# Optimization experiments

Hardware: AMD Instinct MI355X
Metric: run time of the kernel (lower is better)

## Reference

```python
import jax, jax.numpy as jnp
import numpy as np

N = 50000      # nodes
E = 800000     # edges (before self loops)
F_IN = 64      # num_features
HID = 64       # hidden_channels
NCLS = 10      # num_classes
NG = 512       # number of graphs in batch
NEG_SLOPE = 0.2


def setup_inputs() -> dict:
    key = jax.random.key(0)
    ks = jax.random.split(key, 14)
    def g(k, shape, scale=0.1):
        return jax.random.normal(k, shape, dtype=jnp.float32) * scale
    inp = {
        "x": jax.random.normal(ks[0], (N, F_IN), dtype=jnp.float32),
        "edge_index": jax.random.randint(ks[1], (2, E), 0, N, dtype=jnp.int64),
        "batch": jnp.sort(jax.random.randint(ks[2], (N,), 0, NG, dtype=jnp.int64)),
        # conv1: GATv2Conv(F_IN, HID, heads=2), separate lin_l / lin_r, att [H, C]
        "Wl1": g(ks[3], (F_IN, 2 * HID)),
        "Wr1": g(ks[4], (F_IN, 2 * HID)),
        "att1": g(ks[5], (2, HID)),
        "b1": g(ks[6], (2 * HID,)),
        # conv2: GATv2Conv(2*HID, HID, heads=1)
        "Wl2": g(ks[7], (2 * HID, HID)),
        "Wr2": g(ks[8], (2 * HID, HID)),
        "att2": g(ks[9], (1, HID)),
        "b2": g(ks[10], (HID,)),
        # final classifier
        "lin_w": g(ks[11], (HID, NCLS)),
        "lin_b": g(ks[12], (NCLS,)),
    }
    return inp


def _gatv2(x, Wl, Wr, att, b, src, dst, n, heads, outc):
    """GATv2Conv: e = a^T LeakyReLU(Wl x_j + Wr x_i), segment-softmax over dst."""
    xl = (x @ Wl).reshape(n, heads, outc)   # source transform
    xr = (x @ Wr).reshape(n, heads, outc)   # target transform
    e = jax.nn.leaky_relu(xl[src] + xr[dst], NEG_SLOPE)      # [E, H, C]
    logits = jnp.einsum('ehc,hc->eh', e, att)                # [E, H]
    m = jax.lax.stop_gradient(jax.ops.segment_max(logits, dst, num_segments=n))
    ex = jnp.exp(logits - m[dst])
    denom = jax.ops.segment_sum(ex, dst, num_segments=n)     # [N, H]
    alpha = ex / denom[dst]                                  # [E, H]
    out = jax.ops.segment_sum(alpha[:, :, None] * xl[src], dst, num_segments=n)
    return out.reshape(n, heads * outc) + b


def reference(x, edge_index, batch, Wl1, Wr1, att1, b1, Wl2, Wr2, att2, b2, lin_w, lin_b):
    n = x.shape[0]
    loop = jnp.arange(n, dtype=edge_index.dtype)
    src = jnp.concatenate([edge_index[0], loop])   # add_self_loops=True
    dst = jnp.concatenate([edge_index[1], loop])
    h = jax.nn.elu(_gatv2(x, Wl1, Wr1, att1, b1, src, dst, n, 2, HID))   # [N, 2*HID]
    h = _gatv2(h, Wl2, Wr2, att2, b2, src, dst, n, 1, HID)               # [N, HID]
    # global mean pool over graph ids
    sums = jax.ops.segment_sum(h, batch, num_segments=NG)                # [NG, HID]
    cnt = jax.ops.segment_sum(jnp.ones((n,), h.dtype), batch, num_segments=NG)
    pooled = sums / jnp.maximum(cnt, 1.0)[:, None]
    # dropout is identity in eval mode
    return pooled @ lin_w + lin_b                                        # [NG, NCLS]
```

## Files before the change

### kernel.cpp

```cpp
#include <hip/hip_runtime.h>
#include <hip/hip_bf16.h>

#define F_IN 64
#define HID 64
#define NCLS 10
#define NG 512

__global__ void gemm1_kernel(const float* __restrict__ x,
                             const float* __restrict__ Wl,
                             const float* __restrict__ Wr,
                             float* __restrict__ xl, float* __restrict__ xr,
                             int N_) {
    __shared__ float xs[8 * 64];
    int r0 = blockIdx.x * 8;
    int t = threadIdx.x;
    for (int i = t; i < 8 * 64; i += 256) {
        int r = i >> 6;
        xs[i] = (r0 + r < N_) ? x[(long)(r0 + r) * 64 + (i & 63)] : 0.f;
    }
    __syncthreads();
    const float* W = (t < 128) ? Wl : Wr;
    int col = t & 127;
    float acc[8] = {0.f, 0.f, 0.f, 0.f, 0.f, 0.f, 0.f, 0.f};
    for (int k = 0; k < 64; ++k) {
        float w = W[k * 128 + col];
#pragma unroll
        for (int r = 0; r < 8; ++r) acc[r] += xs[r * 64 + k] * w;
    }
    float* out = (t < 128) ? xl : xr;
#pragma unroll
    for (int r = 0; r < 8; ++r)
        if (r0 + r < N_) out[(long)(r0 + r) * 128 + col] = acc[r];
}

__global__ void gemm2_kernel(const float* __restrict__ h1,
                             const float* __restrict__ Wl,
                             const float* __restrict__ Wr,
                             float* __restrict__ xl, float* __restrict__ xr,
                             int N_) {
    __shared__ float hs[8 * 128];
    int r0 = blockIdx.x * 8;
    int t = threadIdx.x;
    for (int i = t; i < 8 * 128; i += 128) {
        int r = i >> 7;
        hs[i] = (r0 + r < N_) ? h1[(long)(r0 + r) * 128 + (i & 127)] : 0.f;
    }
    __syncthreads();
    const float* W = (t < 64) ? Wl : Wr;
    int col = t & 63;
    float acc[8] = {0.f, 0.f, 0.f, 0.f, 0.f, 0.f, 0.f, 0.f};
    for (int k = 0; k < 128; ++k) {
        float w = W[k * 64 + col];
#pragma unroll
        for (int r = 0; r < 8; ++r) acc[r] += hs[r * 128 + k] * w;
    }
    float* out = (t < 64) ? xl : xr;
#pragma unroll
    for (int r = 0; r < 8; ++r)
        if (r0 + r < N_) out[(long)(r0 + r) * 64 + col] = acc[r];
}

__global__ void count_kernel(const int* __restrict__ ei, int* __restrict__ deg, int E_) {
    int e = blockIdx.x * 256 + threadIdx.x;
    if (e < E_) atomicAdd(&deg[ei[E_ + e]], 1);
}

__global__ void scan1_kernel(const int* __restrict__ deg, int* __restrict__ rs_part,
                             int* __restrict__ blksum, int N_) {
    __shared__ int tmp[256];
    int t = threadIdx.x;
    int i = blockIdx.x * 256 + t;
    int v = (i < N_) ? deg[i] : 0;
    tmp[t] = v;
    __syncthreads();
    for (int off = 1; off < 256; off <<= 1) {
        int add = (t >= off) ? tmp[t - off] : 0;
        __syncthreads();
        tmp[t] += add;
        __syncthreads();
    }
    if (i < N_) rs_part[i] = tmp[t] - v;
    if (t == 255) blksum[blockIdx.x] = tmp[255];
}

__global__ void scan2_kernel(int* __restrict__ blksum, int nblk) {
    __shared__ int tmp[256];
    int t = threadIdx.x;
    int v = (t < nblk) ? blksum[t] : 0;
    tmp[t] = v;
    __syncthreads();
    for (int off = 1; off < 256; off <<= 1) {
        int add = (t >= off) ? tmp[t - off] : 0;
        __syncthreads();
        tmp[t] += add;
        __syncthreads();
    }
    if (t < nblk) blksum[t] = tmp[t] - v;
}

__global__ void scan3_kernel(const int* __restrict__ rs_part,
                             const int* __restrict__ blksum,
                             int* __restrict__ rs, int* __restrict__ cursor,
                             int N_, int E_) {
    int i = blockIdx.x * 256 + threadIdx.x;
    if (i < N_) {
        int v = rs_part[i] + blksum[blockIdx.x];
        rs[i] = v;
        cursor[i] = v;
    }
    if (i == 0) rs[N_] = E_;
}

__global__ void scatter_kernel(const int* __restrict__ ei, int* __restrict__ cursor,
                               int* __restrict__ csr_src, int E_) {
    int e = blockIdx.x * 256 + threadIdx.x;
    if (e < E_) {
        int d = ei[E_ + e];
        int pos = atomicAdd(&cursor[d], 1);
        csr_src[pos] = ei[e];
    }
}

__global__ void gbound_kernel(const int* __restrict__ batch, int* __restrict__ gstart,
                              int N_) {
    int i = blockIdx.x * 256 + threadIdx.x;
    if (i >= N_) return;
    int bi = batch[i];
    int bprev = (i == 0) ? -1 : batch[i - 1];
    for (int g = bprev + 1; g <= bi; ++g) gstart[g] = i;
    if (i == N_ - 1)
        for (int g = bi + 1; g <= NG; ++g) gstart[g] = N_;
}

__global__ void gat1_kernel(const float* __restrict__ xl,
                            float* __restrict__ xr,
                            const float* __restrict__ att,
                            const float* __restrict__ b1,
                            const int* __restrict__ rs,
                            const int* __restrict__ csr_src,
                            int N_) {
    int wid = (int)(((long)blockIdx.x * blockDim.x + threadIdx.x) >> 6);
    int lane = threadIdx.x & 63;
    if (wid >= N_ * 2) return;
    int d = wid >> 1, h = wid & 1;
    int g = lane >> 4;
    int c4 = lane & 15;
    long rowoff = (long)d * 128 + h * 64 + c4 * 4;
    const float4 xr4 = *(const float4*)(xr + rowoff);
    const float4 at4 = *(const float4*)(att + h * 64 + c4 * 4);

    int k0 = rs[d], k1 = rs[d + 1];
    int cnt = k1 - k0 + 1;

    float4 acc = make_float4(0.f, 0.f, 0.f, 0.f);
    float den = 0.f;
    for (int c0 = 0; c0 < cnt; c0 += 64) {
        int wl = c0 + lane;
        int myidx = (wl >= 1 && wl < cnt) ? csr_src[k0 + wl - 1] : d;
        int lim = min(64, cnt - c0);
        for (int p = 0; p < lim; p += 8) {
            int e0 = p + g, e1 = p + 4 + g;
            int s0 = __shfl(myidx, e0, 64);
            int s1 = __shfl(myidx, e1, 64);
            bool v0 = e0 < lim, v1 = e1 < lim;
            float4 a0 = *(const float4*)(xl + (long)s0 * 128 + h * 64 + c4 * 4);
            float4 a1 = *(const float4*)(xl + (long)s1 * 128 + h * 64 + c4 * 4);
            float t, p0, p1;
            t = a0.x + xr4.x; t = (t >= 0.f) ? t : 0.2f * t; p0  = at4.x * t;
            t = a0.y + xr4.y; t = (t >= 0.f) ? t : 0.2f * t; p0 += at4.y * t;
            t = a0.z + xr4.z; t = (t >= 0.f) ? t : 0.2f * t; p0 += at4.z * t;
            t = a0.w + xr4.w; t = (t >= 0.f) ? t : 0.2f * t; p0 += at4.w * t;
            t = a1.x + xr4.x; t = (t >= 0.f) ? t : 0.2f * t; p1  = at4.x * t;
            t = a1.y + xr4.y; t = (t >= 0.f) ? t : 0.2f * t; p1 += at4.y * t;
            t = a1.z + xr4.z; t = (t >= 0.f) ? t : 0.2f * t; p1 += at4.z * t;
            t = a1.w + xr4.w; t = (t >= 0.f) ? t : 0.2f * t; p1 += at4.w * t;
            p0 += __shfl_xor(p0, 1, 64);  p1 += __shfl_xor(p1, 1, 64);
            p0 += __shfl_xor(p0, 2, 64);  p1 += __shfl_xor(p1, 2, 64);
            p0 += __shfl_xor(p0, 4, 64);  p1 += __shfl_xor(p1, 4, 64);
            p0 += __shfl_xor(p0, 8, 64);  p1 += __shfl_xor(p1, 8, 64);
            float w0 = v0 ? __expf(p0) : 0.f;
            float w1 = v1 ? __expf(p1) : 0.f;
            acc.x += w0 * a0.x + w1 * a1.x;
            acc.y += w0 * a0.y + w1 * a1.y;
            acc.z += w0 * a0.z + w1 * a1.z;
            acc.w += w0 * a0.w + w1 * a1.w;
            den += w0 + w1;
        }
    }
#pragma unroll
    for (int m = 16; m < 64; m <<= 1) {
        acc.x += __shfl_xor(acc.x, m, 64);
        acc.y += __shfl_xor(acc.y, m, 64);
        acc.z += __shfl_xor(acc.z, m, 64);
        acc.w += __shfl_xor(acc.w, m, 64);
        den   += __shfl_xor(den, m, 64);
    }
    if (g == 0) {
        const float4 b4 = *(const float4*)(b1 + h * 64 + c4 * 4);
        float inv = 1.f / den;
        float4 v;
        v.x = acc.x * inv + b4.x; v.x = (v.x > 0.f) ? v.x : __expf(v.x) - 1.f;
        v.y = acc.y * inv + b4.y; v.y = (v.y > 0.f) ? v.y : __expf(v.y) - 1.f;
        v.z = acc.z * inv + b4.z; v.z = (v.z > 0.f) ? v.z : __expf(v.z) - 1.f;
        v.w = acc.w * inv + b4.w; v.w = (v.w > 0.f) ? v.w : __expf(v.w) - 1.f;
        *(float4*)(xr + rowoff) = v;
    }
}

__global__ void gat2_kernel(const float* __restrict__ xl,
                            const float* __restrict__ xr,
                            const float* __restrict__ att,
                            const float* __restrict__ b2,
                            const int* __restrict__ rs,
                            const int* __restrict__ csr_src,
                            float* __restrict__ h2,
                            int N_) {
    int d = (int)(((long)blockIdx.x * blockDim.x + threadIdx.x) >> 6);
    int lane = threadIdx.x & 63;
    if (d >= N_) return;
    int g = lane >> 4;
    int c4 = lane & 15;
    long rowoff = (long)d * 64 + c4 * 4;
    const float4 xr4 = *(const float4*)(xr + rowoff);
    const float4 at4 = *(const float4*)(att + c4 * 4);

    int k0 = rs[d], k1 = rs[d + 1];
    int cnt = k1 - k0 + 1;

    float4 acc = make_float4(0.f, 0.f, 0.f, 0.f);
    float den = 0.f;
    for (int c0 = 0; c0 < cnt; c0 += 64) {
        int wl = c0 + lane;
        int myidx = (wl >= 1 && wl < cnt) ? csr_src[k0 + wl - 1] : d;
        int lim = min(64, cnt - c0);
        for (int p = 0; p < lim; p += 8) {
            int e0 = p + g, e1 = p + 4 + g;
            int s0 = __shfl(myidx, e0, 64);
            int s1 = __shfl(myidx, e1, 64);
            bool v0 = e0 < lim, v1 = e1 < lim;
            float4 a0 = *(const float4*)(xl + (long)s0 * 64 + c4 * 4);
            float4 a1 = *(const float4*)(xl + (long)s1 * 64 + c4 * 4);
            float t, p0, p1;
            t = a0.x + xr4.x; t = (t >= 0.f) ? t : 0.2f * t; p0  = at4.x * t;
            t = a0.y + xr4.y; t = (t >= 0.f) ? t : 0.2f * t; p0 += at4.y * t;
            t = a0.z + xr4.z; t = (t >= 0.f) ? t : 0.2f * t; p0 += at4.z * t;
            t = a0.w + xr4.w; t = (t >= 0.f) ? t : 0.2f * t; p0 += at4.w * t;
            t = a1.x + xr4.x; t = (t >= 0.f) ? t : 0.2f * t; p1  = at4.x * t;
            t = a1.y + xr4.y; t = (t >= 0.f) ? t : 0.2f * t; p1 += at4.y * t;
            t = a1.z + xr4.z; t = (t >= 0.f) ? t : 0.2f * t; p1 += at4.z * t;
            t = a1.w + xr4.w; t = (t >= 0.f) ? t : 0.2f * t; p1 += at4.w * t;
            p0 += __shfl_xor(p0, 1, 64);  p1 += __shfl_xor(p1, 1, 64);
            p0 += __shfl_xor(p0, 2, 64);  p1 += __shfl_xor(p1, 2, 64);
            p0 += __shfl_xor(p0, 4, 64);  p1 += __shfl_xor(p1, 4, 64);
            p0 += __shfl_xor(p0, 8, 64);  p1 += __shfl_xor(p1, 8, 64);
            float w0 = v0 ? __expf(p0) : 0.f;
            float w1 = v1 ? __expf(p1) : 0.f;
            acc.x += w0 * a0.x + w1 * a1.x;
            acc.y += w0 * a0.y + w1 * a1.y;
            acc.z += w0 * a0.z + w1 * a1.z;
            acc.w += w0 * a0.w + w1 * a1.w;
            den += w0 + w1;
        }
    }
#pragma unroll
    for (int m = 16; m < 64; m <<= 1) {
        acc.x += __shfl_xor(acc.x, m, 64);
        acc.y += __shfl_xor(acc.y, m, 64);
        acc.z += __shfl_xor(acc.z, m, 64);
        acc.w += __shfl_xor(acc.w, m, 64);
        den   += __shfl_xor(den, m, 64);
    }
    if (g == 0) {
        const float4 b4 = *(const float4*)(b2 + c4 * 4);
        float inv = 1.f / den;
        float4 v;
        v.x = acc.x * inv + b4.x;
        v.y = acc.y * inv + b4.y;
        v.z = acc.z * inv + b4.z;
        v.w = acc.w * inv + b4.w;
        *(float4*)(h2 + rowoff) = v;
    }
}

__global__ void pool_final_kernel(const float* __restrict__ h2,
                                  const int* __restrict__ gstart,
                                  const float* __restrict__ lin_w,
                                  const float* __restrict__ lin_b,
                                  float* __restrict__ out) {
    int g = blockIdx.x;
    int lane = threadIdx.x;
    int s = gstart[g], e = gstart[g + 1];
    float acc = 0.f;
    int i = s;
    for (; i + 3 < e; i += 4) {
        float v0 = h2[(long)i * 64 + lane];
        float v1 = h2[(long)(i + 1) * 64 + lane];
        float v2 = h2[(long)(i + 2) * 64 + lane];
        float v3 = h2[(long)(i + 3) * 64 + lane];
        acc += (v0 + v1) + (v2 + v3);
    }
    for (; i < e; ++i) acc += h2[(long)i * 64 + lane];
    float pc = acc / fmaxf((float)(e - s), 1.f);
    __shared__ float pl[64];
    pl[lane] = pc;
    __syncthreads();
    if (lane < NCLS) {
        float o = lin_b[lane];
#pragma unroll 8
        for (int c = 0; c < 64; ++c) o += pl[c] * lin_w[c * NCLS + lane];
        out[g * NCLS + lane] = o;
    }
}

extern "C" void kernel_launch(void* const* d_in, const int* in_sizes, int n_in,
                              void* d_out, int out_size, void* d_ws, size_t ws_size,
                              hipStream_t stream) {
    const float* x     = (const float*)d_in[0];
    const int*   ei    = (const int*)d_in[1];
    const int*   batch = (const int*)d_in[2];
    const float* Wl1   = (const float*)d_in[3];
    const float* Wr1   = (const float*)d_in[4];
    const float* att1  = (const float*)d_in[5];
    const float* b1    = (const float*)d_in[6];
    const float* Wl2   = (const float*)d_in[7];
    const float* Wr2   = (const float*)d_in[8];
    const float* att2  = (const float*)d_in[9];
    const float* b2    = (const float*)d_in[10];
    const float* lin_w = (const float*)d_in[11];
    const float* lin_b = (const float*)d_in[12];
    float* out = (float*)d_out;

    const int N_ = in_sizes[0] / F_IN;
    const int E_ = in_sizes[1] / 2;

    float* ws = (float*)d_ws;
    float* A = ws;
    float* B = A + (long)N_ * 128;
    int* deg     = (int*)(B + (long)N_ * 128);
    int* rs      = deg + N_;
    int* cursor  = rs + N_ + 1;
    int* csr_src = cursor + N_;
    int* gstart  = csr_src + E_;
    int* rs_part = gstart + NG + 1;
    int* blksum  = rs_part + N_;
    float* xl2 = A;
    float* xr2 = A + (long)N_ * 64;
    float* h2  = B;

    const int nblk = (N_ + 255) / 256;

    hipMemsetAsync(deg, 0, (size_t)N_ * sizeof(int), stream);
    count_kernel<<<(E_ + 255) / 256, 256, 0, stream>>>(ei, deg, E_);
    gbound_kernel<<<(N_ + 255) / 256, 256, 0, stream>>>(batch, gstart, N_);
    scan1_kernel<<<nblk, 256, 0, stream>>>(deg, rs_part, blksum, N_);
    scan2_kernel<<<1, 256, 0, stream>>>(blksum, nblk);
    scan3_kernel<<<nblk, 256, 0, stream>>>(rs_part, blksum, rs, cursor, N_, E_);
    scatter_kernel<<<(E_ + 255) / 256, 256, 0, stream>>>(ei, cursor, csr_src, E_);

    gemm1_kernel<<<(N_ + 7) / 8, 256, 0, stream>>>(x, Wl1, Wr1, A, B, N_);
    {
        long waves = (long)N_ * 2;
        int blocks = (int)((waves * 64 + 255) / 256);
        gat1_kernel<<<blocks, 256, 0, stream>>>(A, B, att1, b1, rs, csr_src, N_);
    }

    gemm2_kernel<<<(N_ + 7) / 8, 128, 0, stream>>>(B, Wl2, Wr2, xl2, xr2, N_);
    {
        int blocks = (int)(((long)N_ * 64 + 255) / 256);
        gat2_kernel<<<blocks, 256, 0, stream>>>(xl2, xr2, att2, b2, rs, csr_src, h2, N_);
    }

    pool_final_kernel<<<NG, 64, 0, stream>>>(h2, gstart, lin_w, lin_b, out);
}
```

Measured before the change: 296.4 us.

## Register-tile both GEMMs with float4 and process both GAT1 heads per wave

```diff
diff --git a/kernel.cpp b/kernel.cpp
--- a/kernel.cpp
+++ b/kernel.cpp
@@ -11,26 +11,44 @@
                              const float* __restrict__ Wr,
                              float* __restrict__ xl, float* __restrict__ xr,
                              int N_) {
-    __shared__ float xs[8 * 64];
-    int r0 = blockIdx.x * 8;
+    __shared__ float xs[32 * 64];
+    int r0 = blockIdx.x * 32;
     int t = threadIdx.x;
-    for (int i = t; i < 8 * 64; i += 256) {
-        int r = i >> 6;
-        xs[i] = (r0 + r < N_) ? x[(long)(r0 + r) * 64 + (i & 63)] : 0.f;
+    for (int i = t; i < 512; i += 256) {
+        int row = i >> 4, c4 = i & 15;
+        float4 v = make_float4(0.f, 0.f, 0.f, 0.f);
+        if (r0 + row < N_) v = *(const float4*)(x + (long)(r0 + row) * 64 + c4 * 4);
+        ((float4*)xs)[i] = v;
     }
     __syncthreads();
-    const float* W = (t < 128) ? Wl : Wr;
-    int col = t & 127;
-    float acc[8] = {0.f, 0.f, 0.f, 0.f, 0.f, 0.f, 0.f, 0.f};
+    int rg = t >> 5;
+    int cg = t & 31;
+    float4 accl[4], accr[4];
+#pragma unroll
+    for (int r = 0; r < 4; ++r) {
+        accl[r] = make_float4(0.f, 0.f, 0.f, 0.f);
+        accr[r] = make_float4(0.f, 0.f, 0.f, 0.f);
+    }
     for (int k = 0; k < 64; ++k) {
-        float w = W[k * 128 + col];
-#pragma unroll
-        for (int r = 0; r < 8; ++r) acc[r] += xs[r * 64 + k] * w;
-    }
-    float* out = (t < 128) ? xl : xr;
-#pragma unroll
-    for (int r = 0; r < 8; ++r)
-        if (r0 + r < N_) out[(long)(r0 + r) * 128 + col] = acc[r];
+        float4 wl4 = *(const float4*)(Wl + k * 128 + cg * 4);
+        float4 wr4 = *(const float4*)(Wr + k * 128 + cg * 4);
+#pragma unroll
+        for (int r = 0; r < 4; ++r) {
+            float s = xs[(rg * 4 + r) * 64 + k];
+            accl[r].x += s * wl4.x; accl[r].y += s * wl4.y;
+            accl[r].z += s * wl4.z; accl[r].w += s * wl4.w;
+            accr[r].x += s * wr4.x; accr[r].y += s * wr4.y;
+            accr[r].z += s * wr4.z; accr[r].w += s * wr4.w;
+        }
+    }
+#pragma unroll
+    for (int r = 0; r < 4; ++r) {
+        int row = r0 + rg * 4 + r;
+        if (row < N_) {
+            *(float4*)(xl + (long)row * 128 + cg * 4) = accl[r];
+            *(float4*)(xr + (long)row * 128 + cg * 4) = accr[r];
+        }
+    }
 }
 
 __global__ void gemm2_kernel(const float* __restrict__ h1,
@@ -38,26 +56,44 @@
                              const float* __restrict__ Wr,
                              float* __restrict__ xl, float* __restrict__ xr,
                              int N_) {
-    __shared__ float hs[8 * 128];
-    int r0 = blockIdx.x * 8;
+    __shared__ float hs[32 * 128];
+    int r0 = blockIdx.x * 32;
     int t = threadIdx.x;
-    for (int i = t; i < 8 * 128; i += 128) {
-        int r = i >> 7;
-        hs[i] = (r0 + r < N_) ? h1[(long)(r0 + r) * 128 + (i & 127)] : 0.f;
+    for (int i = t; i < 1024; i += 256) {
+        int row = i >> 5, c4 = i & 31;
+        float4 v = make_float4(0.f, 0.f, 0.f, 0.f);
+        if (r0 + row < N_) v = *(const float4*)(h1 + (long)(r0 + row) * 128 + c4 * 4);
+        ((float4*)hs)[i] = v;
     }
     __syncthreads();
-    const float* W = (t < 64) ? Wl : Wr;
-    int col = t & 63;
-    float acc[8] = {0.f, 0.f, 0.f, 0.f, 0.f, 0.f, 0.f, 0.f};
+    int rg = t >> 4;
+    int cg = t & 15;
+    float4 accl[2], accr[2];
+#pragma unroll
+    for (int r = 0; r < 2; ++r) {
+        accl[r] = make_float4(0.f, 0.f, 0.f, 0.f);
+        accr[r] = make_float4(0.f, 0.f, 0.f, 0.f);
+    }
     for (int k = 0; k < 128; ++k) {
-        float w = W[k * 64 + col];
-#pragma unroll
-        for (int r = 0; r < 8; ++r) acc[r] += hs[r * 128 + k] * w;
-    }
-    float* out = (t < 64) ? xl : xr;
-#pragma unroll
-    for (int r = 0; r < 8; ++r)
-        if (r0 + r < N_) out[(long)(r0 + r) * 64 + col] = acc[r];
+        float4 wl4 = *(const float4*)(Wl + k * 64 + cg * 4);
+        float4 wr4 = *(const float4*)(Wr + k * 64 + cg * 4);
+#pragma unroll
+        for (int r = 0; r < 2; ++r) {
+            float s = hs[(rg * 2 + r) * 128 + k];
+            accl[r].x += s * wl4.x; accl[r].y += s * wl4.y;
+            accl[r].z += s * wl4.z; accl[r].w += s * wl4.w;
+            accr[r].x += s * wr4.x; accr[r].y += s * wr4.y;
+            accr[r].z += s * wr4.z; accr[r].w += s * wr4.w;
+        }
+    }
+#pragma unroll
+    for (int r = 0; r < 2; ++r) {
+        int row = r0 + rg * 2 + r;
+        if (row < N_) {
+            *(float4*)(xl + (long)row * 64 + cg * 4) = accl[r];
+            *(float4*)(xr + (long)row * 64 + cg * 4) = accr[r];
+        }
+    }
 }
 
 __global__ void count_kernel(const int* __restrict__ ei, int* __restrict__ deg, int E_) {
@@ -139,15 +175,14 @@
                             const int* __restrict__ rs,
                             const int* __restrict__ csr_src,
                             int N_) {
-    int wid = (int)(((long)blockIdx.x * blockDim.x + threadIdx.x) >> 6);
+    int d = (int)(((long)blockIdx.x * blockDim.x + threadIdx.x) >> 6);
     int lane = threadIdx.x & 63;
-    if (wid >= N_ * 2) return;
-    int d = wid >> 1, h = wid & 1;
-    int g = lane >> 4;
-    int c4 = lane & 15;
-    long rowoff = (long)d * 128 + h * 64 + c4 * 4;
+    if (d >= N_) return;
+    int slot = lane >> 5;
+    int c8 = lane & 31;
+    long rowoff = (long)d * 128 + c8 * 4;
     const float4 xr4 = *(const float4*)(xr + rowoff);
-    const float4 at4 = *(const float4*)(att + h * 64 + c4 * 4);
+    const float4 at4 = *(const float4*)(att + c8 * 4);
 
     int k0 = rs[d], k1 = rs[d + 1];
     int cnt = k1 - k0 + 1;
@@ -158,22 +193,22 @@
         int wl = c0 + lane;
         int myidx = (wl >= 1 && wl < cnt) ? csr_src[k0 + wl - 1] : d;
         int lim = min(64, cnt - c0);
-        for (int p = 0; p < lim; p += 8) {
-            int e0 = p + g, e1 = p + 4 + g;
+        for (int p = 0; p < lim; p += 4) {
+            int e0 = p + slot, e1 = p + 2 + slot;
             int s0 = __shfl(myidx, e0, 64);
             int s1 = __shfl(myidx, e1, 64);
             bool v0 = e0 < lim, v1 = e1 < lim;
-            float4 a0 = *(const float4*)(xl + (long)s0 * 128 + h * 64 + c4 * 4);
-            float4 a1 = *(const float4*)(xl + (long)s1 * 128 + h * 64 + c4 * 4);
+            float4 a0 = *(const float4*)(xl + (long)s0 * 128 + c8 * 4);
+            float4 a1 = *(const float4*)(xl + (long)s1 * 128 + c8 * 4);
             float t, p0, p1;
-            t = a0.x + xr4.x; t = (t >= 0.f) ? t : 0.2f * t; p0  = at4.x * t;
-            t = a0.y + xr4.y; t = (t >= 0.f) ? t : 0.2f * t; p0 += at4.y * t;
-            t = a0.z + xr4.z; t = (t >= 0.f) ? t : 0.2f * t; p0 += at4.z * t;
-            t = a0.w + xr4.w; t = (t >= 0.f) ? t : 0.2f * t; p0 += at4.w * t;
-            t = a1.x + xr4.x; t = (t >= 0.f) ? t : 0.2f * t; p1  = at4.x * t;
-            t = a1.y + xr4.y; t = (t >= 0.f) ? t : 0.2f * t; p1 += at4.y * t;
-            t = a1.z + xr4.z; t = (t >= 0.f) ? t : 0.2f * t; p1 += at4.z * t;
-            t = a1.w + xr4.w; t = (t >= 0.f) ? t : 0.2f * t; p1 += at4.w * t;
+            t = a0.x + xr4.x; t = fmaxf(t, 0.2f * t); p0  = at4.x * t;
+            t = a0.y + xr4.y; t = fmaxf(t, 0.2f * t); p0 += at4.y * t;
+            t = a0.z + xr4.z; t = fmaxf(t, 0.2f * t); p0 += at4.z * t;
+            t = a0.w + xr4.w; t = fmaxf(t, 0.2f * t); p0 += at4.w * t;
+            t = a1.x + xr4.x; t = fmaxf(t, 0.2f * t); p1  = at4.x * t;
+            t = a1.y + xr4.y; t = fmaxf(t, 0.2f * t); p1 += at4.y * t;
+            t = a1.z + xr4.z; t = fmaxf(t, 0.2f * t); p1 += at4.z * t;
+            t = a1.w + xr4.w; t = fmaxf(t, 0.2f * t); p1 += at4.w * t;
             p0 += __shfl_xor(p0, 1, 64);  p1 += __shfl_xor(p1, 1, 64);
             p0 += __shfl_xor(p0, 2, 64);  p1 += __shfl_xor(p1, 2, 64);
             p0 += __shfl_xor(p0, 4, 64);  p1 += __shfl_xor(p1, 4, 64);
@@ -187,16 +222,13 @@
             den += w0 + w1;
         }
     }
-#pragma unroll
-    for (int m = 16; m < 64; m <<= 1) {
-        acc.x += __shfl_xor(acc.x, m, 64);
-        acc.y += __shfl_xor(acc.y, m, 64);
-        acc.z += __shfl_xor(acc.z, m, 64);
-        acc.w += __shfl_xor(acc.w, m, 64);
-        den   += __shfl_xor(den, m, 64);
-    }
-    if (g == 0) {
-        const float4 b4 = *(const float4*)(b1 + h * 64 + c4 * 4);
+    acc.x += __shfl_xor(acc.x, 32, 64);
+    acc.y += __shfl_xor(acc.y, 32, 64);
+    acc.z += __shfl_xor(acc.z, 32, 64);
+    acc.w += __shfl_xor(acc.w, 32, 64);
+    den   += __shfl_xor(den, 32, 64);
+    if (slot == 0) {
+        const float4 b4 = *(const float4*)(b1 + c8 * 4);
         float inv = 1.f / den;
         float4 v;
         v.x = acc.x * inv + b4.x; v.x = (v.x > 0.f) ? v.x : __expf(v.x) - 1.f;
@@ -241,14 +273,14 @@
             float4 a0 = *(const float4*)(xl + (long)s0 * 64 + c4 * 4);
             float4 a1 = *(const float4*)(xl + (long)s1 * 64 + c4 * 4);
             float t, p0, p1;
-            t = a0.x + xr4.x; t = (t >= 0.f) ? t : 0.2f * t; p0  = at4.x * t;
-            t = a0.y + xr4.y; t = (t >= 0.f) ? t : 0.2f * t; p0 += at4.y * t;
-            t = a0.z + xr4.z; t = (t >= 0.f) ? t : 0.2f * t; p0 += at4.z * t;
-            t = a0.w + xr4.w; t = (t >= 0.f) ? t : 0.2f * t; p0 += at4.w * t;
-            t = a1.x + xr4.x; t = (t >= 0.f) ? t : 0.2f * t; p1  = at4.x * t;
-            t = a1.y + xr4.y; t = (t >= 0.f) ? t : 0.2f * t; p1 += at4.y * t;
-            t = a1.z + xr4.z; t = (t >= 0.f) ? t : 0.2f * t; p1 += at4.z * t;
-            t = a1.w + xr4.w; t = (t >= 0.f) ? t : 0.2f * t; p1 += at4.w * t;
+            t = a0.x + xr4.x; t = fmaxf(t, 0.2f * t); p0  = at4.x * t;
+            t = a0.y + xr4.y; t = fmaxf(t, 0.2f * t); p0 += at4.y * t;
+            t = a0.z + xr4.z; t = fmaxf(t, 0.2f * t); p0 += at4.z * t;
+            t = a0.w + xr4.w; t = fmaxf(t, 0.2f * t); p0 += at4.w * t;
+            t = a1.x + xr4.x; t = fmaxf(t, 0.2f * t); p1  = at4.x * t;
+            t = a1.y + xr4.y; t = fmaxf(t, 0.2f * t); p1 += at4.y * t;
+            t = a1.z + xr4.z; t = fmaxf(t, 0.2f * t); p1 += at4.z * t;
+            t = a1.w + xr4.w; t = fmaxf(t, 0.2f * t); p1 += at4.w * t;
             p0 += __shfl_xor(p0, 1, 64);  p1 += __shfl_xor(p1, 1, 64);
             p0 += __shfl_xor(p0, 2, 64);  p1 += __shfl_xor(p1, 2, 64);
             p0 += __shfl_xor(p0, 4, 64);  p1 += __shfl_xor(p1, 4, 64);
@@ -357,14 +389,13 @@
     scan3_kernel<<<nblk, 256, 0, stream>>>(rs_part, blksum, rs, cursor, N_, E_);
     scatter_kernel<<<(E_ + 255) / 256, 256, 0, stream>>>(ei, cursor, csr_src, E_);
 
-    gemm1_kernel<<<(N_ + 7) / 8, 256, 0, stream>>>(x, Wl1, Wr1, A, B, N_);
+    gemm1_kernel<<<(N_ + 31) / 32, 256, 0, stream>>>(x, Wl1, Wr1, A, B, N_);
     {
-        long waves = (long)N_ * 2;
-        int blocks = (int)((waves * 64 + 255) / 256);
+        int blocks = (int)(((long)N_ * 64 + 255) / 256);
         gat1_kernel<<<blocks, 256, 0, stream>>>(A, B, att1, b1, rs, csr_src, N_);
     }
 
-    gemm2_kernel<<<(N_ + 7) / 8, 128, 0, stream>>>(B, Wl2, Wr2, xl2, xr2, N_);
+    gemm2_kernel<<<(N_ + 31) / 32, 256, 0, stream>>>(B, Wl2, Wr2, xl2, xr2, N_);
     {
         int blocks = (int)(((long)N_ * 64 + 255) / 256);
         gat2_kernel<<<blocks, 256, 0, stream>>>(xl2, xr2, att2, b2, rs, csr_src, h2, N_);
```

Result: slower. 319.7 us (+7.9%).

## Process both attention heads per wavefront in GAT layer 1

Applied to the files above, without the earlier changes.

```diff
diff --git a/kernel.cpp b/kernel.cpp
--- a/kernel.cpp
+++ b/kernel.cpp
@@ -139,15 +139,14 @@
                             const int* __restrict__ rs,
                             const int* __restrict__ csr_src,
                             int N_) {
-    int wid = (int)(((long)blockIdx.x * blockDim.x + threadIdx.x) >> 6);
+    int d = (int)(((long)blockIdx.x * blockDim.x + threadIdx.x) >> 6);
     int lane = threadIdx.x & 63;
-    if (wid >= N_ * 2) return;
-    int d = wid >> 1, h = wid & 1;
-    int g = lane >> 4;
-    int c4 = lane & 15;
-    long rowoff = (long)d * 128 + h * 64 + c4 * 4;
+    if (d >= N_) return;
+    int slot = lane >> 5;
+    int c8 = lane & 31;
+    long rowoff = (long)d * 128 + c8 * 4;
     const float4 xr4 = *(const float4*)(xr + rowoff);
-    const float4 at4 = *(const float4*)(att + h * 64 + c4 * 4);
+    const float4 at4 = *(const float4*)(att + c8 * 4);
 
     int k0 = rs[d], k1 = rs[d + 1];
     int cnt = k1 - k0 + 1;
@@ -158,22 +157,22 @@
         int wl = c0 + lane;
         int myidx = (wl >= 1 && wl < cnt) ? csr_src[k0 + wl - 1] : d;
         int lim = min(64, cnt - c0);
-        for (int p = 0; p < lim; p += 8) {
-            int e0 = p + g, e1 = p + 4 + g;
+        for (int p = 0; p < lim; p += 4) {
+            int e0 = p + slot, e1 = p + 2 + slot;
             int s0 = __shfl(myidx, e0, 64);
             int s1 = __shfl(myidx, e1, 64);
             bool v0 = e0 < lim, v1 = e1 < lim;
-            float4 a0 = *(const float4*)(xl + (long)s0 * 128 + h * 64 + c4 * 4);
-            float4 a1 = *(const float4*)(xl + (long)s1 * 128 + h * 64 + c4 * 4);
+            float4 a0 = *(const float4*)(xl + (long)s0 * 128 + c8 * 4);
+            float4 a1 = *(const float4*)(xl + (long)s1 * 128 + c8 * 4);
             float t, p0, p1;
-            t = a0.x + xr4.x; t = (t >= 0.f) ? t : 0.2f * t; p0  = at4.x * t;
-            t = a0.y + xr4.y; t = (t >= 0.f) ? t : 0.2f * t; p0 += at4.y * t;
-            t = a0.z + xr4.z; t = (t >= 0.f) ? t : 0.2f * t; p0 += at4.z * t;
-            t = a0.w + xr4.w; t = (t >= 0.f) ? t : 0.2f * t; p0 += at4.w * t;
-            t = a1.x + xr4.x; t = (t >= 0.f) ? t : 0.2f * t; p1  = at4.x * t;
-            t = a1.y + xr4.y; t = (t >= 0.f) ? t : 0.2f * t; p1 += at4.y * t;
-            t = a1.z + xr4.z; t = (t >= 0.f) ? t : 0.2f * t; p1 += at4.z * t;
-            t = a1.w + xr4.w; t = (t >= 0.f) ? t : 0.2f * t; p1 += at4.w * t;
+            t = a0.x + xr4.x; t = fmaxf(t, 0.2f * t); p0  = at4.x * t;
+            t = a0.y + xr4.y; t = fmaxf(t, 0.2f * t); p0 += at4.y * t;
+            t = a0.z + xr4.z; t = fmaxf(t, 0.2f * t); p0 += at4.z * t;
+            t = a0.w + xr4.w; t = fmaxf(t, 0.2f * t); p0 += at4.w * t;
+            t = a1.x + xr4.x; t = fmaxf(t, 0.2f * t); p1  = at4.x * t;
+            t = a1.y + xr4.y; t = fmaxf(t, 0.2f * t); p1 += at4.y * t;
+            t = a1.z + xr4.z; t = fmaxf(t, 0.2f * t); p1 += at4.z * t;
+            t = a1.w + xr4.w; t = fmaxf(t, 0.2f * t); p1 += at4.w * t;
             p0 += __shfl_xor(p0, 1, 64);  p1 += __shfl_xor(p1, 1, 64);
             p0 += __shfl_xor(p0, 2, 64);  p1 += __shfl_xor(p1, 2, 64);
             p0 += __shfl_xor(p0, 4, 64);  p1 += __shfl_xor(p1, 4, 64);
@@ -187,16 +186,13 @@
             den += w0 + w1;
         }
     }
-#pragma unroll
-    for (int m = 16; m < 64; m <<= 1) {
-        acc.x += __shfl_xor(acc.x, m, 64);
-        acc.y += __shfl_xor(acc.y, m, 64);
-        acc.z += __shfl_xor(acc.z, m, 64);
-        acc.w += __shfl_xor(acc.w, m, 64);
-        den   += __shfl_xor(den, m, 64);
-    }
-    if (g == 0) {
-        const float4 b4 = *(const float4*)(b1 + h * 64 + c4 * 4);
+    acc.x += __shfl_xor(acc.x, 32, 64);
+    acc.y += __shfl_xor(acc.y, 32, 64);
+    acc.z += __shfl_xor(acc.z, 32, 64);
+    acc.w += __shfl_xor(acc.w, 32, 64);
+    den   += __shfl_xor(den, 32, 64);
+    if (slot == 0) {
+        const float4 b4 = *(const float4*)(b1 + c8 * 4);
         float inv = 1.f / den;
         float4 v;
         v.x = acc.x * inv + b4.x; v.x = (v.x > 0.f) ? v.x : __expf(v.x) - 1.f;
@@ -241,14 +237,14 @@
             float4 a0 = *(const float4*)(xl + (long)s0 * 64 + c4 * 4);
             float4 a1 = *(const float4*)(xl + (long)s1 * 64 + c4 * 4);
             float t, p0, p1;
-            t = a0.x + xr4.x; t = (t >= 0.f) ? t : 0.2f * t; p0  = at4.x * t;
-            t = a0.y + xr4.y; t = (t >= 0.f) ? t : 0.2f * t; p0 += at4.y * t;
-            t = a0.z + xr4.z; t = (t >= 0.f) ? t : 0.2f * t; p0 += at4.z * t;
-            t = a0.w + xr4.w; t = (t >= 0.f) ? t : 0.2f * t; p0 += at4.w * t;
-            t = a1.x + xr4.x; t = (t >= 0.f) ? t : 0.2f * t; p1  = at4.x * t;
-            t = a1.y + xr4.y; t = (t >= 0.f) ? t : 0.2f * t; p1 += at4.y * t;
-            t = a1.z + xr4.z; t = (t >= 0.f) ? t : 0.2f * t; p1 += at4.z * t;
-            t = a1.w + xr4.w; t = (t >= 0.f) ? t : 0.2f * t; p1 += at4.w * t;
+            t = a0.x + xr4.x; t = fmaxf(t, 0.2f * t); p0  = at4.x * t;
+            t = a0.y + xr4.y; t = fmaxf(t, 0.2f * t); p0 += at4.y * t;
+            t = a0.z + xr4.z; t = fmaxf(t, 0.2f * t); p0 += at4.z * t;
+            t = a0.w + xr4.w; t = fmaxf(t, 0.2f * t); p0 += at4.w * t;
+            t = a1.x + xr4.x; t = fmaxf(t, 0.2f * t); p1  = at4.x * t;
+            t = a1.y + xr4.y; t = fmaxf(t, 0.2f * t); p1 += at4.y * t;
+            t = a1.z + xr4.z; t = fmaxf(t, 0.2f * t); p1 += at4.z * t;
+            t = a1.w + xr4.w; t = fmaxf(t, 0.2f * t); p1 += at4.w * t;
             p0 += __shfl_xor(p0, 1, 64);  p1 += __shfl_xor(p1, 1, 64);
             p0 += __shfl_xor(p0, 2, 64);  p1 += __shfl_xor(p1, 2, 64);
             p0 += __shfl_xor(p0, 4, 64);  p1 += __shfl_xor(p1, 4, 64);
@@ -359,8 +355,7 @@
 
     gemm1_kernel<<<(N_ + 7) / 8, 256, 0, stream>>>(x, Wl1, Wr1, A, B, N_);
     {
-        long waves = (long)N_ * 2;
-        int blocks = (int)((waves * 64 + 255) / 256);
+        int blocks = (int)(((long)N_ * 64 + 255) / 256);
         gat1_kernel<<<blocks, 256, 0, stream>>>(A, B, att1, b1, rs, csr_src, N_);
     }
 
```

Result: no change. 297.1 us (+0.2%).
